# Optimization experiments

Hardware: AMD Instinct MI355X
Metric: run time of the kernel (lower is better)

## Reference

```python
import jax, jax.numpy as jnp
import numpy as np

HEADS = 16
DIM_HEAD = 64
SCALE = DIM_HEAD ** -0.5
EPS = 1e-5


def _bitlinear(x, w):
    """BitNet b1.58 BitLinear (kyegomez/BitNet), eval-mode, bias-free.
    w: [out, in] torch-layout. Ternary weight quant (scale = mean|w|),
    per-token int8 absmax activation quant, straight-through estimator.
    """
    ws = 1.0 / jnp.clip(jnp.mean(jnp.abs(w)), EPS, None)
    wq = jnp.clip(jnp.round(w * ws), -1.0, 1.0) / ws
    wq = w + jax.lax.stop_gradient(wq - w)
    xs = 127.0 / jnp.clip(jnp.max(jnp.abs(x), axis=-1, keepdims=True), EPS, None)
    xq = jnp.clip(jnp.round(x * xs), -128.0, 127.0) / xs
    xq = x + jax.lax.stop_gradient(xq - x)
    return jnp.einsum('bnd,od->bno', xq, wq)


def setup_inputs() -> dict:
    key = jax.random.key(0)
    ks = jax.random.split(key, 6)
    b, n, d = 2, 2048, 1024
    return {
        'x': jax.random.normal(ks[0], (b, n, d), dtype=jnp.float32),
        'context': jax.random.normal(ks[1], (b, n, d), dtype=jnp.float32),
        'Wq': jax.random.normal(ks[2], (d, d), dtype=jnp.float32) * 0.02,
        'Wk': jax.random.normal(ks[3], (d, d), dtype=jnp.float32) * 0.02,
        'Wv': jax.random.normal(ks[4], (d, d), dtype=jnp.float32) * 0.02,
        'Wo': jax.random.normal(ks[5], (d, d), dtype=jnp.float32) * 0.02,
    }


def reference(x, context, Wq, Wk, Wv, Wo):
    b, n, _ = x.shape
    m = context.shape[1]
    q = _bitlinear(x, Wq)
    k = _bitlinear(context, Wk)
    v = _bitlinear(context, Wv)
    # b n (h d) -> b h n d
    q = q.reshape(b, n, HEADS, DIM_HEAD).transpose(0, 2, 1, 3)
    k = k.reshape(b, m, HEADS, DIM_HEAD).transpose(0, 2, 1, 3)
    v = v.reshape(b, m, HEADS, DIM_HEAD).transpose(0, 2, 1, 3)
    dots = jnp.einsum('bhid,bhjd->bhij', q, k) * SCALE
    attn = jax.nn.softmax(dots, axis=-1)  # dropout is identity in eval
    out = jnp.einsum('bhij,bhjd->bhid', attn, v)
    out = out.transpose(0, 2, 1, 3).reshape(b, n, HEADS * DIM_HEAD)
    return _bitlinear(out, Wo)
```

## Files before the change

kernel.cpp:

```cpp
#include <hip/hip_runtime.h>
#include <math.h>

#define HEADS   16
#define DHEAD   64
#define SEQ     2048
#define NB      2
#define DM      1024
#define NTOK    4096
#define WEPS    1e-5

using bf16x8  = __attribute__((ext_vector_type(8))) __bf16;
using f16x8   = __attribute__((ext_vector_type(8))) _Float16;
using floatx4 = __attribute__((ext_vector_type(4))) float;

typedef __attribute__((address_space(1))) unsigned int gu32;
typedef __attribute__((address_space(3))) unsigned int lu32;

__device__ __forceinline__ unsigned short f32_bf16_bits(float f) {
    union { float f; unsigned u; } cv; cv.f = f;
    return (unsigned short)(cv.u >> 16);
}

__device__ __forceinline__ unsigned pack2(_Float16 a, _Float16 b) {
    union { _Float16 h[2]; unsigned u; } c; c.h[0] = a; c.h[1] = b; return c.u;
}
__device__ __forceinline__ _Float16 lo16(unsigned u) {
    union { unsigned u; _Float16 h[2]; } c; c.u = u; return c.h[0];
}
__device__ __forceinline__ _Float16 hi16(unsigned u) {
    union { unsigned u; _Float16 h[2]; } c; c.u = u; return c.h[1];
}

__global__ void wsum1(const float* __restrict__ w0, const float* __restrict__ w1,
                      const float* __restrict__ w2, const float* __restrict__ w3,
                      double* __restrict__ partial) {
    const float* w = (blockIdx.y == 0) ? w0 : (blockIdx.y == 1) ? w1 : (blockIdx.y == 2) ? w2 : w3;
    int base = blockIdx.x * 16384;
    double s = 0.0;
    for (int i = threadIdx.x; i < 16384; i += 256)
        s += fabs((double)w[base + i]);
    __shared__ double sd[256];
    sd[threadIdx.x] = s;
    __syncthreads();
    for (int st = 128; st > 0; st >>= 1) {
        if (threadIdx.x < st) sd[threadIdx.x] += sd[threadIdx.x + st];
        __syncthreads();
    }
    if (threadIdx.x == 0) partial[blockIdx.y * 64 + blockIdx.x] = sd[0];
}

__global__ void wsum2(const double* __restrict__ partial, double* __restrict__ wscale) {
    int t = threadIdx.x;
    if (t < 4) {
        double s = 0.0;
        for (int i = 0; i < 64; i++) s += partial[t * 64 + i];
        double mean = s / (1024.0 * 1024.0);
        wscale[t] = (mean > WEPS) ? mean : WEPS;
    }
}

__global__ void wquant(const float* __restrict__ w0, const float* __restrict__ w1,
                       const float* __restrict__ w2, const float* __restrict__ w3,
                       const double* __restrict__ wscale, unsigned short* __restrict__ wq) {
    int widx = blockIdx.y;
    const float* w = (widx == 0) ? w0 : (widx == 1) ? w1 : (widx == 2) ? w2 : w3;
    double ws = 1.0 / wscale[widx];
    int idx = (blockIdx.x * 256 + threadIdx.x) * 4;
    float4 wv = *(const float4*)(w + idx);
    ushort4 o;
    {
        double r = rint((double)wv.x * ws); r = r > 1.0 ? 1.0 : (r < -1.0 ? -1.0 : r); o.x = f32_bf16_bits((float)r);
    } {
        double r = rint((double)wv.y * ws); r = r > 1.0 ? 1.0 : (r < -1.0 ? -1.0 : r); o.y = f32_bf16_bits((float)r);
    } {
        double r = rint((double)wv.z * ws); r = r > 1.0 ? 1.0 : (r < -1.0 ? -1.0 : r); o.z = f32_bf16_bits((float)r);
    } {
        double r = rint((double)wv.w * ws); r = r > 1.0 ? 1.0 : (r < -1.0 ? -1.0 : r); o.w = f32_bf16_bits((float)r);
    }
    *(ushort4*)(wq + (size_t)widx * 1048576 + idx) = o;
}

__device__ __forceinline__ void aquant_row(const float* __restrict__ row,
                                           unsigned short* __restrict__ dst_row,
                                           double* __restrict__ ascale_p) {
    int t = threadIdx.x;
    float4 xv = *(const float4*)(row + t * 4);
    float a = fmaxf(fmaxf(fabsf(xv.x), fabsf(xv.y)), fmaxf(fabsf(xv.z), fabsf(xv.w)));
    __shared__ float sm[256];
    sm[t] = a;
    __syncthreads();
    for (int st = 128; st > 0; st >>= 1) {
        if (t < st) sm[t] = fmaxf(sm[t], sm[t + st]);
        __syncthreads();
    }
    double mx = (double)sm[0];
    if (mx < WEPS) mx = WEPS;
    if (t == 0) *ascale_p = mx / 127.0;
    double xs = 127.0 / mx;
    ushort4 o;
    {
        double r = rint((double)xv.x * xs); r = r > 127.0 ? 127.0 : (r < -128.0 ? -128.0 : r); o.x = f32_bf16_bits((float)r);
    } {
        double r = rint((double)xv.y * xs); r = r > 127.0 ? 127.0 : (r < -128.0 ? -128.0 : r); o.y = f32_bf16_bits((float)r);
    } {
        double r = rint((double)xv.z * xs); r = r > 127.0 ? 127.0 : (r < -128.0 ? -128.0 : r); o.z = f32_bf16_bits((float)r);
    } {
        double r = rint((double)xv.w * xs); r = r > 127.0 ? 127.0 : (r < -128.0 ? -128.0 : r); o.w = f32_bf16_bits((float)r);
    }
    *(ushort4*)(dst_row + t * 4) = o;
}

__global__ void aquant(const float* __restrict__ src, unsigned short* __restrict__ dst,
                       double* __restrict__ ascale) {
    int tok = blockIdx.x;
    aquant_row(src + (size_t)tok * DM, dst + (size_t)tok * DM, ascale + tok);
}

__global__ void aquant2(const float* __restrict__ x, const float* __restrict__ ctx,
                        unsigned short* __restrict__ dst, double* __restrict__ ascale) {
    int tok = blockIdx.x;
    const float* row = (tok < NTOK) ? x + (size_t)tok * DM : ctx + (size_t)(tok - NTOK) * DM;
    aquant_row(row, dst + (size_t)tok * DM, ascale + tok);
}

__device__ __forceinline__ void gemm_core(
        const unsigned short* __restrict__ A, const unsigned short* __restrict__ W,
        const double* __restrict__ ascale, double wsc,
        void* __restrict__ outp, int mode, float prescale, int bx, int by) {
    __shared__ unsigned short lds_a[128 * 32];
    __shared__ unsigned short lds_b[128 * 32];
    const int tid  = threadIdx.x;
    const int wave = tid >> 6, lane = tid & 63;
    const int wr = wave >> 1, wc = wave & 1;
    const int quad = lane >> 4, l15 = lane & 15;
    const int row0 = by * 128, col0 = bx * 128;
    floatx4 acc[4][4] = {};

    const unsigned short* ga0 = A + (size_t)(row0 + (lane >> 2)) * DM + (lane & 3) * 8;
    const unsigned short* gb0 = W + (size_t)(col0 + (lane >> 2)) * DM + (lane & 3) * 8;

    for (int k0 = 0; k0 < DM; k0 += 32) {
        __syncthreads();
        #pragma unroll
        for (int t = 0; t < 2; t++) {
            const int i = wave + t * 4;
            __builtin_amdgcn_global_load_lds(
                (const gu32*)(const void*)(ga0 + (size_t)i * 16 * DM + k0),
                (lu32*)(void*)(lds_a + i * 512), 16, 0, 0);
            __builtin_amdgcn_global_load_lds(
                (const gu32*)(const void*)(gb0 + (size_t)i * 16 * DM + k0),
                (lu32*)(void*)(lds_b + i * 512), 16, 0, 0);
        }
        __syncthreads();
        bf16x8 af[4], bfr[4];
        #pragma unroll
        for (int mi = 0; mi < 4; mi++) {
            int r = wr * 64 + mi * 16 + l15;
            af[mi] = *(const bf16x8*)&lds_a[r * 32 + quad * 8];
        }
        #pragma unroll
        for (int ni = 0; ni < 4; ni++) {
            int n = wc * 64 + ni * 16 + l15;
            bfr[ni] = *(const bf16x8*)&lds_b[n * 32 + quad * 8];
        }
        #pragma unroll
        for (int mi = 0; mi < 4; mi++)
            #pragma unroll
            for (int ni = 0; ni < 4; ni++)
                acc[mi][ni] = __builtin_amdgcn_mfma_f32_16x16x32_bf16(af[mi], bfr[ni], acc[mi][ni], 0, 0, 0);
    }

    #pragma unroll
    for (int mi = 0; mi < 4; mi++) {
        int tbase = row0 + wr * 64 + mi * 16 + quad * 4;
        #pragma unroll
        for (int reg = 0; reg < 4; reg++) {
            int t = tbase + reg;
            double sa = ascale[t] * wsc;
            #pragma unroll
            for (int ni = 0; ni < 4; ni++) {
                int o = col0 + wc * 64 + ni * 16 + l15;
                float val = (float)((double)acc[mi][ni][reg] * sa);
                if (mode == 0) {
                    int bb = t >> 11, n = t & 2047, hh = o >> 6, dh = o & 63;
                    float fv = val * prescale;
                    _Float16 hl = (_Float16)fv;
                    _Float16 ml = (_Float16)((fv - (float)hl) * 2048.0f);
                    ((unsigned*)outp)[(((size_t)(bb * HEADS + hh) * SEQ + n) << 6) + dh] = pack2(hl, ml);
                } else {
                    ((float*)outp)[(size_t)t * DM + o] = val;
                }
            }
        }
    }
}

__global__ __launch_bounds__(256) void gemm_qkv(
        const unsigned short* __restrict__ xq, const unsigned short* __restrict__ cq,
        const unsigned short* __restrict__ wqb, const double* __restrict__ ascale_x,
        const double* __restrict__ wscale, unsigned* __restrict__ qkv) {
    const int which = blockIdx.x >> 3;
    gemm_core(which == 0 ? xq : cq,
              wqb + (size_t)which * 1048576,
              ascale_x + (which ? NTOK : 0),
              wscale[which],
              qkv + (size_t)which * 4194304,
              0, which == 0 ? 0.125f : 1.0f, blockIdx.x & 7, blockIdx.y);
}

__global__ __launch_bounds__(256) void gemm_o(
        const unsigned short* __restrict__ aq, const unsigned short* __restrict__ wo,
        const double* __restrict__ ascale, const double* __restrict__ wscale_p,
        float* __restrict__ out) {
    gemm_core(aq, wo, ascale, *wscale_p, out, 1, 1.0f, blockIdx.x, blockIdx.y);
}

#define KH_IDX(row, d8) (((row) * 8 + ((d8) ^ ((row) & 7))) * 8)
#define VT_IDX(row, kc) (((row) * 8 + ((kc) ^ ((row) & 7))) * 4)
#define PP_IDX(row, kc) (((row) * 8 + ((kc) ^ ((row) & 7))) * 4)

__global__ __launch_bounds__(256, 2) void attn_mfma(
        const unsigned* __restrict__ qg, const unsigned* __restrict__ kg,
        const unsigned* __restrict__ vg, float* __restrict__ out) {
    __shared__ __align__(16) _Float16 Kh[32 * 64];
    __shared__ __align__(16) _Float16 Kl[32 * 64];
    __shared__ __align__(16) unsigned Vt[64 * 32];
    __shared__ __align__(16) unsigned Pp[4][32 * 32];
    __shared__ float Lp[4][2][16][4];

    const int bh   = blockIdx.y;
    const int tid  = threadIdx.x;
    const int wave = tid >> 6, lane = tid & 63;
    const int l15  = lane & 15, quad = lane >> 4;
    const int qbase = blockIdx.x * 128 + wave * 32;

    f16x8 qh[2][2], qm[2][2];
    #pragma unroll
    for (int qs = 0; qs < 2; qs++) {
        #pragma unroll
        for (int c = 0; c < 2; c++) {
            const unsigned* qp = qg + (((size_t)bh * SEQ + qbase + qs * 16 + l15) << 6) + c * 32 + quad * 8;
            uint4 a = *(const uint4*)qp;
            uint4 b = *(const uint4*)(qp + 4);
            unsigned wd[8] = {a.x, a.y, a.z, a.w, b.x, b.y, b.z, b.w};
            #pragma unroll
            for (int j = 0; j < 8; j++) {
                qh[qs][c][j] = lo16(wd[j]);
                qm[qs][c][j] = hi16(wd[j]);
            }
        }
    }

    floatx4 och[2][4] = {};
    floatx4 ocm[2][4] = {};
    float lsum[2] = {0.f, 0.f};

    const unsigned* kbase = kg + ((size_t)bh * SEQ << 6);
    const unsigned* vbase = vg + ((size_t)bh * SEQ << 6);

    for (int kt = 0; kt < SEQ; kt += 32) {
        __syncthreads();
        {
            int kk = tid >> 3, d8 = tid & 7;
            const unsigned* kp = kbase + (((size_t)(kt + kk)) << 6) + d8 * 8;
            uint4 a = *(const uint4*)kp, b = *(const uint4*)(kp + 4);
            unsigned wd[8] = {a.x, a.y, a.z, a.w, b.x, b.y, b.z, b.w};
            f16x8 hv, lv;
            #pragma unroll
            for (int j = 0; j < 8; j++) { hv[j] = lo16(wd[j]); lv[j] = hi16(wd[j]); }
            *(f16x8*)&Kh[KH_IDX(kk, d8)] = hv;
            *(f16x8*)&Kl[KH_IDX(kk, d8)] = lv;
        }
        {
            int key = tid & 31, d0 = (tid >> 5) * 8;
            const unsigned* vp = vbase + (((size_t)(kt + key)) << 6) + d0;
            uint4 a = *(const uint4*)vp, b = *(const uint4*)(vp + 4);
            unsigned wd[8] = {a.x, a.y, a.z, a.w, b.x, b.y, b.z, b.w};
            #pragma unroll
            for (int j = 0; j < 8; j++)
                Vt[VT_IDX(d0 + j, key >> 2) + (key & 3)] = wd[j];
        }
        __syncthreads();

        f16x8 kfh[2][2], kfl[2][2];
        #pragma unroll
        for (int ms = 0; ms < 2; ms++) {
            #pragma unroll
            for (int c = 0; c < 2; c++) {
                kfh[ms][c] = *(const f16x8*)&Kh[KH_IDX(ms * 16 + l15, c * 4 + quad)];
                kfl[ms][c] = *(const f16x8*)&Kl[KH_IDX(ms * 16 + l15, c * 4 + quad)];
            }
        }

        #pragma unroll
        for (int qs = 0; qs < 2; qs++) {
            #pragma unroll
            for (int ms = 0; ms < 2; ms++) {
                floatx4 ah = {}, am = {};
                #pragma unroll
                for (int c = 0; c < 2; c++) {
                    ah = __builtin_amdgcn_mfma_f32_16x16x32_f16(kfh[ms][c], qh[qs][c], ah, 0, 0, 0);
                    am = __builtin_amdgcn_mfma_f32_16x16x32_f16(kfh[ms][c], qm[qs][c], am, 0, 0, 0);
                    am = __builtin_amdgcn_mfma_f32_16x16x32_f16(kfl[ms][c], qh[qs][c], am, 0, 0, 0);
                }
                float p[4];
                #pragma unroll
                for (int r = 0; r < 4; r++) {
                    float s = ah[r] + am[r] * 4.8828125e-4f;
                    p[r] = __expf(s);
                    lsum[qs] += p[r];
                }
                uint4 w;
                {
                    _Float16 h0 = (_Float16)p[0], m0 = (_Float16)((p[0] - (float)h0) * 2048.0f);
                    _Float16 h1 = (_Float16)p[1], m1 = (_Float16)((p[1] - (float)h1) * 2048.0f);
                    _Float16 h2 = (_Float16)p[2], m2 = (_Float16)((p[2] - (float)h2) * 2048.0f);
                    _Float16 h3 = (_Float16)p[3], m3 = (_Float16)((p[3] - (float)h3) * 2048.0f);
                    w.x = pack2(h0, m0); w.y = pack2(h1, m1);
                    w.z = pack2(h2, m2); w.w = pack2(h3, m3);
                }
                *(uint4*)&Pp[wave][PP_IDX(qs * 16 + l15, ms * 4 + quad)] = w;
            }
        }
        __threadfence_block();

        f16x8 vfh[4], vfm[4];
        #pragma unroll
        for (int nh = 0; nh < 4; nh++) {
            uint4 r0 = *(const uint4*)&Vt[VT_IDX(nh * 16 + l15, 2 * quad)];
            uint4 r1 = *(const uint4*)&Vt[VT_IDX(nh * 16 + l15, 2 * quad + 1)];
            unsigned wd[8] = {r0.x, r0.y, r0.z, r0.w, r1.x, r1.y, r1.z, r1.w};
            #pragma unroll
            for (int j = 0; j < 8; j++) { vfh[nh][j] = lo16(wd[j]); vfm[nh][j] = hi16(wd[j]); }
        }
        #pragma unroll
        for (int qs = 0; qs < 2; qs++) {
            uint4 r0 = *(const uint4*)&Pp[wave][PP_IDX(qs * 16 + l15, 2 * quad)];
            uint4 r1 = *(const uint4*)&Pp[wave][PP_IDX(qs * 16 + l15, 2 * quad + 1)];
            unsigned wd[8] = {r0.x, r0.y, r0.z, r0.w, r1.x, r1.y, r1.z, r1.w};
            f16x8 pfh, pfm;
            #pragma unroll
            for (int j = 0; j < 8; j++) { pfh[j] = lo16(wd[j]); pfm[j] = hi16(wd[j]); }
            #pragma unroll
            for (int nh = 0; nh < 4; nh++) {
                och[qs][nh] = __builtin_amdgcn_mfma_f32_16x16x32_f16(pfh, vfh[nh], och[qs][nh], 0, 0, 0);
                ocm[qs][nh] = __builtin_amdgcn_mfma_f32_16x16x32_f16(pfh, vfm[nh], ocm[qs][nh], 0, 0, 0);
                ocm[qs][nh] = __builtin_amdgcn_mfma_f32_16x16x32_f16(pfm, vfh[nh], ocm[qs][nh], 0, 0, 0);
            }
        }
    }

    Lp[wave][0][l15][quad] = lsum[0];
    Lp[wave][1][l15][quad] = lsum[1];
    __threadfence_block();

    int b = bh >> 4, h = bh & 15;
    #pragma unroll
    for (int qs = 0; qs < 2; qs++) {
        float linv[4];
        #pragma unroll
        for (int r = 0; r < 4; r++) {
            float4 lv = *(const float4*)&Lp[wave][qs][quad * 4 + r][0];
            linv[r] = 1.0f / (lv.x + lv.y + lv.z + lv.w);
        }
        #pragma unroll
        for (int nh = 0; nh < 4; nh++) {
            #pragma unroll
            for (int r = 0; r < 4; r++) {
                int token = b * SEQ + qbase + qs * 16 + quad * 4 + r;
                float val = (och[qs][nh][r] + ocm[qs][nh][r] * 4.8828125e-4f) * linv[r];
                out[(size_t)token * DM + h * 64 + nh * 16 + l15] = val;
            }
        }
    }
}

extern "C" void kernel_launch(void* const* d_in, const int* in_sizes, int n_in,
                              void* d_out, int out_size, void* d_ws, size_t ws_size,
                              hipStream_t stream) {
    const float* x       = (const float*)d_in[0];
    const float* context = (const float*)d_in[1];
    const float* Wq      = (const float*)d_in[2];
    const float* Wk      = (const float*)d_in[3];
    const float* Wv      = (const float*)d_in[4];
    const float* Wo      = (const float*)d_in[5];
    char* ws = (char*)d_ws;

    double* wscale   = (double*)(ws + 0);
    double* partial  = (double*)(ws + 4096);
    double* ascale_x = (double*)(ws + 8192);
    double* ascale_a = (double*)(ws + 73728);
    unsigned short* wqb = (unsigned short*)(ws + 131072);
    unsigned short* xq  = (unsigned short*)(ws + 8519680);
    unsigned short* cq  = (unsigned short*)(ws + 16908288);
    float* attn_out = (float*)(ws + 8519680);
    unsigned* qkvp = (unsigned*)(ws + 25296896);
    unsigned short* aq = (unsigned short*)(ws + 25296896);

    wsum1<<<dim3(64, 4), 256, 0, stream>>>(Wq, Wk, Wv, Wo, partial);
    wsum2<<<1, 64, 0, stream>>>(partial, wscale);
    wquant<<<dim3(1024, 4), 256, 0, stream>>>(Wq, Wk, Wv, Wo, wscale, wqb);
    aquant2<<<2 * NTOK, 256, 0, stream>>>(x, context, xq, ascale_x);

    gemm_qkv<<<dim3(24, 32), 256, 0, stream>>>(xq, cq, wqb, ascale_x, wscale, qkvp);

    attn_mfma<<<dim3(16, 32), 256, 0, stream>>>(qkvp, qkvp + 4194304, qkvp + 8388608, attn_out);

    aquant<<<NTOK, 256, 0, stream>>>(attn_out, aq, ascale_a);
    gemm_o<<<dim3(8, 32), 256, 0, stream>>>(aq, wqb + 3145728, ascale_a, wscale + 3, (float*)d_out);
}
```

Measured before the change: 332.4 us.

## Switch BitLinear GEMMs to int8 MFMA and store V transposed for attention

Ternary weights and quantized activations are now stored as int8 instead of bf16, and the projection GEMMs use the i32 16x16x64 int8 MFMA with a K step of 64. This halves operand bytes and doubles the K depth per instruction, and exact integer accumulation keeps the results correct. Separately, the QKV GEMM epilogue writes V in a transposed (d-major) layout. The attention kernel then loads V fragments straight from global into registers, dropping the per-tile LDS transpose and one shared buffer. The cost is strided global stores in the V epilogue.

```diff
diff --git a/kernel.cpp b/kernel.cpp
--- a/kernel.cpp
+++ b/kernel.cpp
@@ -9,17 +9,12 @@
 #define NTOK    4096
 #define WEPS    1e-5
 
-using bf16x8  = __attribute__((ext_vector_type(8))) __bf16;
 using f16x8   = __attribute__((ext_vector_type(8))) _Float16;
 using floatx4 = __attribute__((ext_vector_type(4))) float;
+using i32x4   = __attribute__((ext_vector_type(4))) int;
 
 typedef __attribute__((address_space(1))) unsigned int gu32;
 typedef __attribute__((address_space(3))) unsigned int lu32;
-
-__device__ __forceinline__ unsigned short f32_bf16_bits(float f) {
-    union { float f; unsigned u; } cv; cv.f = f;
-    return (unsigned short)(cv.u >> 16);
-}
 
 __device__ __forceinline__ unsigned pack2(_Float16 a, _Float16 b) {
     union { _Float16 h[2]; unsigned u; } c; c.h[0] = a; c.h[1] = b; return c.u;
@@ -61,27 +56,27 @@
 
 __global__ void wquant(const float* __restrict__ w0, const float* __restrict__ w1,
                        const float* __restrict__ w2, const float* __restrict__ w3,
-                       const double* __restrict__ wscale, unsigned short* __restrict__ wq) {
+                       const double* __restrict__ wscale, signed char* __restrict__ wq) {
     int widx = blockIdx.y;
     const float* w = (widx == 0) ? w0 : (widx == 1) ? w1 : (widx == 2) ? w2 : w3;
     double ws = 1.0 / wscale[widx];
     int idx = (blockIdx.x * 256 + threadIdx.x) * 4;
     float4 wv = *(const float4*)(w + idx);
-    ushort4 o;
+    char4 o;
     {
-        double r = rint((double)wv.x * ws); r = r > 1.0 ? 1.0 : (r < -1.0 ? -1.0 : r); o.x = f32_bf16_bits((float)r);
-    } {
-        double r = rint((double)wv.y * ws); r = r > 1.0 ? 1.0 : (r < -1.0 ? -1.0 : r); o.y = f32_bf16_bits((float)r);
-    } {
-        double r = rint((double)wv.z * ws); r = r > 1.0 ? 1.0 : (r < -1.0 ? -1.0 : r); o.z = f32_bf16_bits((float)r);
-    } {
-        double r = rint((double)wv.w * ws); r = r > 1.0 ? 1.0 : (r < -1.0 ? -1.0 : r); o.w = f32_bf16_bits((float)r);
-    }
-    *(ushort4*)(wq + (size_t)widx * 1048576 + idx) = o;
+        double r = rint((double)wv.x * ws); r = r > 1.0 ? 1.0 : (r < -1.0 ? -1.0 : r); o.x = (signed char)r;
+    } {
+        double r = rint((double)wv.y * ws); r = r > 1.0 ? 1.0 : (r < -1.0 ? -1.0 : r); o.y = (signed char)r;
+    } {
+        double r = rint((double)wv.z * ws); r = r > 1.0 ? 1.0 : (r < -1.0 ? -1.0 : r); o.z = (signed char)r;
+    } {
+        double r = rint((double)wv.w * ws); r = r > 1.0 ? 1.0 : (r < -1.0 ? -1.0 : r); o.w = (signed char)r;
+    }
+    *(char4*)(wq + (size_t)widx * 1048576 + idx) = o;
 }
 
 __device__ __forceinline__ void aquant_row(const float* __restrict__ row,
-                                           unsigned short* __restrict__ dst_row,
+                                           signed char* __restrict__ dst_row,
                                            double* __restrict__ ascale_p) {
     int t = threadIdx.x;
     float4 xv = *(const float4*)(row + t * 4);
@@ -97,77 +92,77 @@
     if (mx < WEPS) mx = WEPS;
     if (t == 0) *ascale_p = mx / 127.0;
     double xs = 127.0 / mx;
-    ushort4 o;
+    char4 o;
     {
-        double r = rint((double)xv.x * xs); r = r > 127.0 ? 127.0 : (r < -128.0 ? -128.0 : r); o.x = f32_bf16_bits((float)r);
-    } {
-        double r = rint((double)xv.y * xs); r = r > 127.0 ? 127.0 : (r < -128.0 ? -128.0 : r); o.y = f32_bf16_bits((float)r);
-    } {
-        double r = rint((double)xv.z * xs); r = r > 127.0 ? 127.0 : (r < -128.0 ? -128.0 : r); o.z = f32_bf16_bits((float)r);
-    } {
-        double r = rint((double)xv.w * xs); r = r > 127.0 ? 127.0 : (r < -128.0 ? -128.0 : r); o.w = f32_bf16_bits((float)r);
-    }
-    *(ushort4*)(dst_row + t * 4) = o;
-}
-
-__global__ void aquant(const float* __restrict__ src, unsigned short* __restrict__ dst,
+        double r = rint((double)xv.x * xs); r = r > 127.0 ? 127.0 : (r < -128.0 ? -128.0 : r); o.x = (signed char)r;
+    } {
+        double r = rint((double)xv.y * xs); r = r > 127.0 ? 127.0 : (r < -128.0 ? -128.0 : r); o.y = (signed char)r;
+    } {
+        double r = rint((double)xv.z * xs); r = r > 127.0 ? 127.0 : (r < -128.0 ? -128.0 : r); o.z = (signed char)r;
+    } {
+        double r = rint((double)xv.w * xs); r = r > 127.0 ? 127.0 : (r < -128.0 ? -128.0 : r); o.w = (signed char)r;
+    }
+    *(char4*)(dst_row + t * 4) = o;
+}
+
+__global__ void aquant(const float* __restrict__ src, signed char* __restrict__ dst,
                        double* __restrict__ ascale) {
     int tok = blockIdx.x;
     aquant_row(src + (size_t)tok * DM, dst + (size_t)tok * DM, ascale + tok);
 }
 
 __global__ void aquant2(const float* __restrict__ x, const float* __restrict__ ctx,
-                        unsigned short* __restrict__ dst, double* __restrict__ ascale) {
+                        signed char* __restrict__ dst, double* __restrict__ ascale) {
     int tok = blockIdx.x;
     const float* row = (tok < NTOK) ? x + (size_t)tok * DM : ctx + (size_t)(tok - NTOK) * DM;
     aquant_row(row, dst + (size_t)tok * DM, ascale + tok);
 }
 
 __device__ __forceinline__ void gemm_core(
-        const unsigned short* __restrict__ A, const unsigned short* __restrict__ W,
+        const signed char* __restrict__ A, const signed char* __restrict__ W,
         const double* __restrict__ ascale, double wsc,
         void* __restrict__ outp, int mode, float prescale, int bx, int by) {
-    __shared__ unsigned short lds_a[128 * 32];
-    __shared__ unsigned short lds_b[128 * 32];
+    __shared__ __align__(16) signed char lds_a[128 * 64];
+    __shared__ __align__(16) signed char lds_b[128 * 64];
     const int tid  = threadIdx.x;
     const int wave = tid >> 6, lane = tid & 63;
     const int wr = wave >> 1, wc = wave & 1;
     const int quad = lane >> 4, l15 = lane & 15;
     const int row0 = by * 128, col0 = bx * 128;
-    floatx4 acc[4][4] = {};
-
-    const unsigned short* ga0 = A + (size_t)(row0 + (lane >> 2)) * DM + (lane & 3) * 8;
-    const unsigned short* gb0 = W + (size_t)(col0 + (lane >> 2)) * DM + (lane & 3) * 8;
-
-    for (int k0 = 0; k0 < DM; k0 += 32) {
+    i32x4 acc[4][4] = {};
+
+    const signed char* ga0 = A + (size_t)(row0 + (lane >> 2)) * DM + (lane & 3) * 16;
+    const signed char* gb0 = W + (size_t)(col0 + (lane >> 2)) * DM + (lane & 3) * 16;
+
+    for (int k0 = 0; k0 < DM; k0 += 64) {
         __syncthreads();
         #pragma unroll
         for (int t = 0; t < 2; t++) {
             const int i = wave + t * 4;
             __builtin_amdgcn_global_load_lds(
                 (const gu32*)(const void*)(ga0 + (size_t)i * 16 * DM + k0),
-                (lu32*)(void*)(lds_a + i * 512), 16, 0, 0);
+                (lu32*)(void*)(lds_a + i * 1024), 16, 0, 0);
             __builtin_amdgcn_global_load_lds(
                 (const gu32*)(const void*)(gb0 + (size_t)i * 16 * DM + k0),
-                (lu32*)(void*)(lds_b + i * 512), 16, 0, 0);
-        }
-        __syncthreads();
-        bf16x8 af[4], bfr[4];
+                (lu32*)(void*)(lds_b + i * 1024), 16, 0, 0);
+        }
+        __syncthreads();
+        i32x4 af[4], bfr[4];
         #pragma unroll
         for (int mi = 0; mi < 4; mi++) {
             int r = wr * 64 + mi * 16 + l15;
-            af[mi] = *(const bf16x8*)&lds_a[r * 32 + quad * 8];
+            af[mi] = *(const i32x4*)&lds_a[r * 64 + quad * 16];
         }
         #pragma unroll
         for (int ni = 0; ni < 4; ni++) {
             int n = wc * 64 + ni * 16 + l15;
-            bfr[ni] = *(const bf16x8*)&lds_b[n * 32 + quad * 8];
+            bfr[ni] = *(const i32x4*)&lds_b[n * 64 + quad * 16];
         }
         #pragma unroll
         for (int mi = 0; mi < 4; mi++)
             #pragma unroll
             for (int ni = 0; ni < 4; ni++)
-                acc[mi][ni] = __builtin_amdgcn_mfma_f32_16x16x32_bf16(af[mi], bfr[ni], acc[mi][ni], 0, 0, 0);
+                acc[mi][ni] = __builtin_amdgcn_mfma_i32_16x16x64_i8(af[mi], bfr[ni], acc[mi][ni], 0, 0, 0);
     }
 
     #pragma unroll
@@ -181,14 +176,18 @@
             for (int ni = 0; ni < 4; ni++) {
                 int o = col0 + wc * 64 + ni * 16 + l15;
                 float val = (float)((double)acc[mi][ni][reg] * sa);
-                if (mode == 0) {
+                if (mode == 1) {
+                    ((float*)outp)[(size_t)t * DM + o] = val;
+                } else {
                     int bb = t >> 11, n = t & 2047, hh = o >> 6, dh = o & 63;
                     float fv = val * prescale;
                     _Float16 hl = (_Float16)fv;
                     _Float16 ml = (_Float16)((fv - (float)hl) * 2048.0f);
-                    ((unsigned*)outp)[(((size_t)(bb * HEADS + hh) * SEQ + n) << 6) + dh] = pack2(hl, ml);
-                } else {
-                    ((float*)outp)[(size_t)t * DM + o] = val;
+                    unsigned pw = pack2(hl, ml);
+                    if (mode == 0)
+                        ((unsigned*)outp)[(((size_t)(bb * HEADS + hh) * SEQ + n) << 6) + dh] = pw;
+                    else
+                        ((unsigned*)outp)[(((size_t)(bb * HEADS + hh) * 64 + dh) << 11) + n] = pw;
                 }
             }
         }
@@ -196,8 +195,8 @@
 }
 
 __global__ __launch_bounds__(256) void gemm_qkv(
-        const unsigned short* __restrict__ xq, const unsigned short* __restrict__ cq,
-        const unsigned short* __restrict__ wqb, const double* __restrict__ ascale_x,
+        const signed char* __restrict__ xq, const signed char* __restrict__ cq,
+        const signed char* __restrict__ wqb, const double* __restrict__ ascale_x,
         const double* __restrict__ wscale, unsigned* __restrict__ qkv) {
     const int which = blockIdx.x >> 3;
     gemm_core(which == 0 ? xq : cq,
@@ -205,18 +204,18 @@
               ascale_x + (which ? NTOK : 0),
               wscale[which],
               qkv + (size_t)which * 4194304,
-              0, which == 0 ? 0.125f : 1.0f, blockIdx.x & 7, blockIdx.y);
+              which == 2 ? 2 : 0,
+              which == 0 ? 0.125f : 1.0f, blockIdx.x & 7, blockIdx.y);
 }
 
 __global__ __launch_bounds__(256) void gemm_o(
-        const unsigned short* __restrict__ aq, const unsigned short* __restrict__ wo,
+        const signed char* __restrict__ aq, const signed char* __restrict__ wo,
         const double* __restrict__ ascale, const double* __restrict__ wscale_p,
         float* __restrict__ out) {
     gemm_core(aq, wo, ascale, *wscale_p, out, 1, 1.0f, blockIdx.x, blockIdx.y);
 }
 
 #define KH_IDX(row, d8) (((row) * 8 + ((d8) ^ ((row) & 7))) * 8)
-#define VT_IDX(row, kc) (((row) * 8 + ((kc) ^ ((row) & 7))) * 4)
 #define PP_IDX(row, kc) (((row) * 8 + ((kc) ^ ((row) & 7))) * 4)
 
 __global__ __launch_bounds__(256, 2) void attn_mfma(
@@ -224,7 +223,6 @@
         const unsigned* __restrict__ vg, float* __restrict__ out) {
     __shared__ __align__(16) _Float16 Kh[32 * 64];
     __shared__ __align__(16) _Float16 Kl[32 * 64];
-    __shared__ __align__(16) unsigned Vt[64 * 32];
     __shared__ __align__(16) unsigned Pp[4][32 * 32];
     __shared__ float Lp[4][2][16][4];
 
@@ -256,9 +254,16 @@
     float lsum[2] = {0.f, 0.f};
 
     const unsigned* kbase = kg + ((size_t)bh * SEQ << 6);
-    const unsigned* vbase = vg + ((size_t)bh * SEQ << 6);
+    const unsigned* vbase = vg + ((size_t)bh << 17);
 
     for (int kt = 0; kt < SEQ; kt += 32) {
+        uint4 va[4], vb[4];
+        #pragma unroll
+        for (int nh = 0; nh < 4; nh++) {
+            const unsigned* vp = vbase + (((size_t)(nh * 16 + l15)) << 11) + kt + quad * 8;
+            va[nh] = *(const uint4*)vp;
+            vb[nh] = *(const uint4*)(vp + 4);
+        }
         __syncthreads();
         {
             int kk = tid >> 3, d8 = tid & 7;
@@ -270,15 +275,6 @@
             for (int j = 0; j < 8; j++) { hv[j] = lo16(wd[j]); lv[j] = hi16(wd[j]); }
             *(f16x8*)&Kh[KH_IDX(kk, d8)] = hv;
             *(f16x8*)&Kl[KH_IDX(kk, d8)] = lv;
-        }
-        {
-            int key = tid & 31, d0 = (tid >> 5) * 8;
-            const unsigned* vp = vbase + (((size_t)(kt + key)) << 6) + d0;
-            uint4 a = *(const uint4*)vp, b = *(const uint4*)(vp + 4);
-            unsigned wd[8] = {a.x, a.y, a.z, a.w, b.x, b.y, b.z, b.w};
-            #pragma unroll
-            for (int j = 0; j < 8; j++)
-                Vt[VT_IDX(d0 + j, key >> 2) + (key & 3)] = wd[j];
         }
         __syncthreads();
 
@@ -327,9 +323,8 @@
         f16x8 vfh[4], vfm[4];
         #pragma unroll
         for (int nh = 0; nh < 4; nh++) {
-            uint4 r0 = *(const uint4*)&Vt[VT_IDX(nh * 16 + l15, 2 * quad)];
-            uint4 r1 = *(const uint4*)&Vt[VT_IDX(nh * 16 + l15, 2 * quad + 1)];
-            unsigned wd[8] = {r0.x, r0.y, r0.z, r0.w, r1.x, r1.y, r1.z, r1.w};
+            unsigned wd[8] = {va[nh].x, va[nh].y, va[nh].z, va[nh].w,
+                              vb[nh].x, vb[nh].y, vb[nh].z, vb[nh].w};
             #pragma unroll
             for (int j = 0; j < 8; j++) { vfh[nh][j] = lo16(wd[j]); vfm[nh][j] = hi16(wd[j]); }
         }
@@ -390,12 +385,12 @@
     double* partial  = (double*)(ws + 4096);
     double* ascale_x = (double*)(ws + 8192);
     double* ascale_a = (double*)(ws + 73728);
-    unsigned short* wqb = (unsigned short*)(ws + 131072);
-    unsigned short* xq  = (unsigned short*)(ws + 8519680);
-    unsigned short* cq  = (unsigned short*)(ws + 16908288);
-    float* attn_out = (float*)(ws + 8519680);
-    unsigned* qkvp = (unsigned*)(ws + 25296896);
-    unsigned short* aq = (unsigned short*)(ws + 25296896);
+    signed char* wqb = (signed char*)(ws + 131072);
+    signed char* xq  = (signed char*)(ws + 4325376);
+    signed char* cq  = (signed char*)(ws + 8519680);
+    float* attn_out  = (float*)(ws + 4325376);
+    unsigned* qkvp   = (unsigned*)(ws + 21102592);
+    signed char* aq  = (signed char*)(ws + 21102592);
 
     wsum1<<<dim3(64, 4), 256, 0, stream>>>(Wq, Wk, Wv, Wo, partial);
     wsum2<<<1, 64, 0, stream>>>(partial, wscale);
```

Result: faster. 315.8 us (-5.0%).
